# Performance work log

Hardware: AMD Instinct MI355X
Metric: run time of the kernel (lower is better)

The kernel has to match this reference:

```python
import jax, jax.numpy as jnp
import numpy as np

N_STEPS = 16
T_FINAL = 1.0


def setup_inputs() -> dict:
    key = jax.random.key(0)
    k = jax.random.split(key, 5)
    B, n, S = 131072, 8, 1
    return {
        "U0": jax.random.normal(k[0], (B, n, n), jnp.float32),
        "eps": jax.random.normal(k[1], (S, B, n, n), jnp.float32),
        "W0": 0.1 * jax.random.normal(k[2], (n, n), jnp.float32),
        "W1": 0.1 * jax.random.normal(k[3], (n, n), jnp.float32),
        "W2": 0.1 * jax.random.normal(k[4], (n, n), jnp.float32),
    }


def _alg_dyn(t, U, W0, W1, W2):
    # F(t, U; p) = antisym(W0 + t*W1 + U W2 U^T)  (real anti-Hermitian part)
    M = W0 + t * W1 + jnp.einsum('bij,jk,blk->bil', U, W2, U)
    return 0.5 * (M - jnp.swapaxes(M, -1, -2))


def _vel(t, U, W0, W1, W2):
    # dU/dt = F(t, U) @ U
    return _alg_dyn(t, U, W0, W1, W2) @ U


def _logj_rate(t, U, eps, W0, W1, W2):
    # Hutchinson estimator of tr(d vel / dU) per batch element: E_v[v . J v]
    f = lambda u: _vel(t, u, W0, W1, W2)

    def one(v):
        _, jv = jax.jvp(f, (U,), (v,))
        return jnp.sum(v * jv, axis=(-2, -1))  # [B]

    return jnp.mean(jax.vmap(one)(eps), axis=0)  # [B]


def reference(U0, eps, W0, W1, W2):
    dt = T_FINAL / N_STEPS

    def rhs(t, U):
        return _vel(t, U, W0, W1, W2), _logj_rate(t, U, eps, W0, W1, W2)

    def step(carry, i):
        U, lj = carry
        t = i.astype(U.dtype) * dt
        k1u, k1l = rhs(t, U)
        k2u, k2l = rhs(t + 0.5 * dt, U + 0.5 * dt * k1u)
        k3u, k3l = rhs(t + 0.5 * dt, U + 0.5 * dt * k2u)
        k4u, k4l = rhs(t + dt, U + dt * k3u)
        U = U + (dt / 6.0) * (k1u + 2.0 * k2u + 2.0 * k3u + k4u)
        lj = lj + (dt / 6.0) * (k1l + 2.0 * k2l + 2.0 * k3l + k4l)
        return (U, lj), None

    logj0 = jnp.zeros((U0.shape[0],), U0.dtype)
    (U, logj), _ = jax.lax.scan(step, (U0, logj0), jnp.arange(N_STEPS))
    return U, logj
```

## Files before the change

kernel.cpp:

```cpp
#include <hip/hip_runtime.h>
#include <stdint.h>

typedef unsigned int u32;
typedef unsigned short u16;
typedef float v2f __attribute__((ext_vector_type(2)));

#define NSTEP 16
#define DTS (1.0f/16.0f)

#define TAB_FLAG 0
#define TAB_W2   8
#define TAB_W2M  72
#define TAB_WT   136

__device__ __forceinline__ float b2f(u16 h){ return __uint_as_float(((u32)h) << 16); }
__device__ __forceinline__ u32 f2b(float f){
  u32 u = __float_as_uint(f);
  return (u + 0x7fffu + ((u >> 16) & 1u)) >> 16;
}
__host__ __device__ constexpr int TRI(int i, int j){ return i*7 - (i*(i-1))/2 + (j-i-1); }

__global__ void prep_kernel(const void* __restrict__ W0v, const void* __restrict__ W1v,
                            const void* __restrict__ W2v, float* __restrict__ ws)
{
  __shared__ int sflag;
  __shared__ float sW0[64], sW1[64], sW2[64];
  int t = threadIdx.x;

  if (t == 0) {
    const u16* w2h = (const u16*)W2v;
    int ok = 1;
    for (int x = 0; x < 64; ++x) {
      float v = b2f(w2h[x]);
      if (!(v > -1024.0f && v < 1024.0f)) { ok = 0; break; }
    }
    sflag = ok;
    ws[TAB_FLAG] = (float)ok;
  }
  __syncthreads();
  int isbf = sflag;

  if (t < 64) {
    if (isbf) {
      sW0[t] = b2f(((const u16*)W0v)[t]);
      sW1[t] = b2f(((const u16*)W1v)[t]);
      sW2[t] = b2f(((const u16*)W2v)[t]);
    } else {
      sW0[t] = ((const float*)W0v)[t];
      sW1[t] = ((const float*)W1v)[t];
      sW2[t] = ((const float*)W2v)[t];
    }
  }
  __syncthreads();

  if (t < 64) {
    int i = t >> 3, j = t & 7;
    ws[TAB_W2  + t] = sW2[t];
    ws[TAB_W2M + t] = sW2[t] - sW2[j*8+i];
  }
  for (int idx = t; idx < 64*28; idx += 256) {
    int s = idx / 28;
    int e = idx - s*28;
    int i = 0, r = e;
    while (r >= 7 - i) { r -= 7 - i; ++i; }
    int j = i + 1 + r;
    int step = s >> 2, st = s & 3;
    float toff = (st == 0) ? 0.0f : ((st == 3) ? 1.0f : 0.5f);
    float tt = ((float)step + toff) * DTS;
    float w0a = 0.5f*(sW0[i*8+j] - sW0[j*8+i]);
    float w1a = 0.5f*(sW1[i*8+j] - sW1[j*8+i]);
    ws[TAB_WT + s*32 + e] = fmaf(tt, w1a, w0a);
  }
}

#define SC(arr,i,k) (((k)&1) ? arr[(i)*4+((k)>>1)].y : arr[(i)*4+((k)>>1)].x)

__global__ void __attribute__((amdgpu_flat_work_group_size(256,256), amdgpu_waves_per_eu(1,1)))
flow_kernel(const void* __restrict__ U0v, const void* __restrict__ EPSv,
            const float* __restrict__ ws, void* __restrict__ outv, int B)
{
  int b = blockIdx.x * 256 + threadIdx.x;
  if (b >= B) return;
  const int isbf = (ws[TAB_FLAG] != 0.0f);

  v2f U2[32], V2[32], E2[32];
  if (isbf) {
    const uint4* pu = (const uint4*)((const u16*)U0v + (size_t)b*64);
    const uint4* pv = (const uint4*)((const u16*)EPSv + (size_t)b*64);
    #pragma unroll
    for (int q = 0; q < 8; ++q) {
      uint4 xu = pu[q];
      uint4 xv = pv[q];
      U2[4*q+0] = (v2f){b2f((u16)(xu.x&0xffffu)), b2f((u16)(xu.x>>16))};
      U2[4*q+1] = (v2f){b2f((u16)(xu.y&0xffffu)), b2f((u16)(xu.y>>16))};
      U2[4*q+2] = (v2f){b2f((u16)(xu.z&0xffffu)), b2f((u16)(xu.z>>16))};
      U2[4*q+3] = (v2f){b2f((u16)(xu.w&0xffffu)), b2f((u16)(xu.w>>16))};
      V2[4*q+0] = (v2f){b2f((u16)(xv.x&0xffffu)), b2f((u16)(xv.x>>16))};
      V2[4*q+1] = (v2f){b2f((u16)(xv.y&0xffffu)), b2f((u16)(xv.y>>16))};
      V2[4*q+2] = (v2f){b2f((u16)(xv.z&0xffffu)), b2f((u16)(xv.z>>16))};
      V2[4*q+3] = (v2f){b2f((u16)(xv.w&0xffffu)), b2f((u16)(xv.w>>16))};
    }
  } else {
    const float4* pu = (const float4*)((const float*)U0v + (size_t)b*64);
    const float4* pv = (const float4*)((const float*)EPSv + (size_t)b*64);
    #pragma unroll
    for (int q = 0; q < 16; ++q) {
      float4 xu = pu[q];
      float4 xv = pv[q];
      U2[2*q+0] = (v2f){xu.x, xu.y};  U2[2*q+1] = (v2f){xu.z, xu.w};
      V2[2*q+0] = (v2f){xv.x, xv.y};  V2[2*q+1] = (v2f){xv.z, xv.w};
    }
  }

  const v2f* W2p  = (const v2f*)(ws + TAB_W2);
  const v2f* W2mp = (const v2f*)(ws + TAB_W2M);

  #pragma unroll
  for (int i = 0; i < 8; ++i) {
    #pragma unroll
    for (int jp = 0; jp < 4; ++jp) {
      v2f a = SC(V2,i,0) * W2mp[0*4+jp];
      #pragma unroll
      for (int k = 1; k < 8; ++k) a += SC(V2,i,k) * W2mp[k*4+jp];
      E2[i*4+jp] = a;
    }
  }

  float lj = 0.0f;

  #pragma unroll 1
  for (int step = 0; step < NSTEP; ++step) {
    v2f Us2[32], acc2[32];
    #pragma unroll
    for (int x = 0; x < 32; ++x) { Us2[x] = U2[x]; acc2[x] = (v2f){0.0f, 0.0f}; }

    #pragma unroll 1
    for (int stage = 0; stage < 4; ++stage) {
      const float* wt = ws + TAB_WT + (size_t)(((step << 2) | stage) << 5);

      v2f A2[32];
      #pragma unroll
      for (int i = 0; i < 8; ++i) {
        #pragma unroll
        for (int jp = 0; jp < 4; ++jp) {
          v2f a = SC(U2,i,0) * W2p[0*4+jp];
          #pragma unroll
          for (int k = 1; k < 8; ++k) a += SC(U2,i,k) * W2p[k*4+jp];
          A2[i*4+jp] = a;
        }
      }

      float Fu[28];
      #pragma unroll
      for (int i = 0; i < 8; ++i) {
        #pragma unroll
        for (int j = i+1; j < 8; ++j) {
          v2f s2 = A2[i*4+0] * U2[j*4+0];
          #pragma unroll
          for (int kp = 1; kp < 4; ++kp) s2 += A2[i*4+kp] * U2[j*4+kp];
          #pragma unroll
          for (int kp = 0; kp < 4; ++kp) s2 -= A2[j*4+kp] * U2[i*4+kp];
          Fu[TRI(i,j)] = fmaf(0.5f, s2.x + s2.y, wt[TRI(i,j)]);
        }
      }

      float Ssum = 0.0f;
      #pragma unroll
      for (int i = 0; i < 8; ++i) {
        #pragma unroll
        for (int j = i+1; j < 8; ++j) {
          v2f d2 = V2[i*4+0] * U2[j*4+0];
          #pragma unroll
          for (int kp = 1; kp < 4; ++kp) d2 += V2[i*4+kp] * U2[j*4+kp];
          #pragma unroll
          for (int kp = 0; kp < 4; ++kp) d2 -= U2[i*4+kp] * V2[j*4+kp];
          v2f g2 = E2[i*4+0] * U2[j*4+0];
          #pragma unroll
          for (int kp = 1; kp < 4; ++kp) g2 += E2[i*4+kp] * U2[j*4+kp];
          #pragma unroll
          for (int kp = 0; kp < 4; ++kp) g2 -= E2[j*4+kp] * U2[i*4+kp];
          Ssum = fmaf(d2.x + d2.y, g2.x + g2.y, Ssum);
        }
      }
      float cl = (stage == 1 || stage == 2) ? (DTS/6.0f) : (DTS/12.0f);
      lj = fmaf(cl, Ssum, lj);

      float wa = (stage == 1 || stage == 2) ? 2.0f : 1.0f;
      #pragma unroll
      for (int i = 0; i < 8; ++i) {
        #pragma unroll
        for (int jp = 0; jp < 4; ++jp) {
          const int k0 = (i == 0) ? 1 : 0;
          float f0 = (i < k0) ? Fu[TRI(i<k0?i:k0, i<k0?k0:i)] : -Fu[TRI(i<k0?i:k0, i<k0?k0:i)];
          v2f s2 = f0 * U2[k0*4+jp];
          #pragma unroll
          for (int k = 0; k < 8; ++k) {
            if (k == i || k == k0) continue;
            float fk = (i < k) ? Fu[TRI(i<k?i:k, i<k?k:i)] : -Fu[TRI(i<k?i:k, i<k?k:i)];
            s2 += fk * U2[k*4+jp];
          }
          A2[i*4+jp] = s2;
          acc2[i*4+jp] += wa * s2;
        }
      }
      if (stage < 3) {
        float cs = (stage == 2) ? DTS : (0.5f*DTS);
        #pragma unroll
        for (int x = 0; x < 32; ++x) U2[x] = Us2[x] + cs * A2[x];
      }
    }

    #pragma unroll
    for (int x = 0; x < 32; ++x) U2[x] = Us2[x] + (DTS/6.0f) * acc2[x];
  }

  if (isbf) {
    u16* outU = (u16*)outv;
    uint4* po = (uint4*)(outU + (size_t)b*64);
    #pragma unroll
    for (int q = 0; q < 8; ++q) {
      uint4 o;
      o.x = f2b(U2[4*q+0].x) | (f2b(U2[4*q+0].y) << 16);
      o.y = f2b(U2[4*q+1].x) | (f2b(U2[4*q+1].y) << 16);
      o.z = f2b(U2[4*q+2].x) | (f2b(U2[4*q+2].y) << 16);
      o.w = f2b(U2[4*q+3].x) | (f2b(U2[4*q+3].y) << 16);
      po[q] = o;
    }
    outU[(size_t)B*64 + b] = (u16)f2b(lj);
  } else {
    float* outU = (float*)outv;
    float4* po = (float4*)(outU + (size_t)b*64);
    #pragma unroll
    for (int q = 0; q < 16; ++q) {
      float4 o;
      o.x = U2[2*q].x; o.y = U2[2*q].y; o.z = U2[2*q+1].x; o.w = U2[2*q+1].y;
      po[q] = o;
    }
    outU[(size_t)B*64 + b] = lj;
  }
}

extern "C" void kernel_launch(void* const* d_in, const int* in_sizes, int n_in,
                              void* d_out, int out_size, void* d_ws, size_t ws_size,
                              hipStream_t stream) {
  const void* U0  = d_in[0];
  const void* EPS = d_in[1];
  const void* W0  = d_in[2];
  const void* W1  = d_in[3];
  const void* W2  = d_in[4];
  float* ws = (float*)d_ws;
  int B = in_sizes[0] / 64;

  hipLaunchKernelGGL(prep_kernel, dim3(1), dim3(256), 0, stream, W0, W1, W2, ws);
  hipLaunchKernelGGL(flow_kernel, dim3((B + 255) / 256), dim3(256), 0, stream,
                     U0, EPS, ws, d_out, B);
}
```

Before: 629.2 us.

## Move V and E to LDS as bf16, restructure dots for register pressure

```diff
diff --git a/kernel.cpp b/kernel.cpp
--- a/kernel.cpp
+++ b/kernel.cpp
@@ -14,11 +14,22 @@
 #define TAB_WT   136
 
 __device__ __forceinline__ float b2f(u16 h){ return __uint_as_float(((u32)h) << 16); }
+__device__ __forceinline__ float bflo(u32 w){ return __uint_as_float(w << 16); }
+__device__ __forceinline__ float bfhi(u32 w){ return __uint_as_float(w & 0xffff0000u); }
 __device__ __forceinline__ u32 f2b(float f){
   u32 u = __float_as_uint(f);
   return (u + 0x7fffu + ((u >> 16) & 1u)) >> 16;
 }
 __host__ __device__ constexpr int TRI(int i, int j){ return i*7 - (i*(i-1))/2 + (j-i-1); }
+
+__device__ __forceinline__ v2f vfma(v2f a, v2f b, v2f c){ return __builtin_elementwise_fma(a, b, c); }
+__device__ __forceinline__ float dot8(const v2f* a, const v2f* u){
+  v2f d = a[0] * u[0];
+  d = vfma(a[1], u[1], d);
+  d = vfma(a[2], u[2], d);
+  d = vfma(a[3], u[3], d);
+  return d.x + d.y;
+}
 
 __global__ void prep_kernel(const void* __restrict__ W0v, const void* __restrict__ W1v,
                             const void* __restrict__ W2v, float* __restrict__ ws)
@@ -73,32 +84,57 @@
   }
 }
 
-#define SC(arr,i,k) (((k)&1) ? arr[(i)*4+((k)>>1)].y : arr[(i)*4+((k)>>1)].x)
-
-__global__ void __attribute__((amdgpu_flat_work_group_size(256,256), amdgpu_waves_per_eu(1,1)))
-flow_kernel(const void* __restrict__ U0v, const void* __restrict__ EPSv,
-            const float* __restrict__ ws, void* __restrict__ outv, int B)
+__global__ __launch_bounds__(256, 2) void flow_kernel(
+    const void* __restrict__ U0v, const void* __restrict__ EPSv,
+    const float* __restrict__ ws, void* __restrict__ outv, int B)
 {
-  int b = blockIdx.x * 256 + threadIdx.x;
+  __shared__ uint4 sV[8][256];
+  __shared__ uint4 sE[8][256];
+
+  const int tid = threadIdx.x;
+  const int b = blockIdx.x * 256 + tid;
   if (b >= B) return;
   const int isbf = (ws[TAB_FLAG] != 0.0f);
 
-  v2f U2[32], V2[32], E2[32];
+  const v2f* W2p = (const v2f*)(ws + TAB_W2);
+  const v2f* Mp  = (const v2f*)(ws + TAB_W2M);
+
+  v2f U2[32];
+
   if (isbf) {
     const uint4* pu = (const uint4*)((const u16*)U0v + (size_t)b*64);
     const uint4* pv = (const uint4*)((const u16*)EPSv + (size_t)b*64);
     #pragma unroll
     for (int q = 0; q < 8; ++q) {
       uint4 xu = pu[q];
-      uint4 xv = pv[q];
-      U2[4*q+0] = (v2f){b2f((u16)(xu.x&0xffffu)), b2f((u16)(xu.x>>16))};
-      U2[4*q+1] = (v2f){b2f((u16)(xu.y&0xffffu)), b2f((u16)(xu.y>>16))};
-      U2[4*q+2] = (v2f){b2f((u16)(xu.z&0xffffu)), b2f((u16)(xu.z>>16))};
-      U2[4*q+3] = (v2f){b2f((u16)(xu.w&0xffffu)), b2f((u16)(xu.w>>16))};
-      V2[4*q+0] = (v2f){b2f((u16)(xv.x&0xffffu)), b2f((u16)(xv.x>>16))};
-      V2[4*q+1] = (v2f){b2f((u16)(xv.y&0xffffu)), b2f((u16)(xv.y>>16))};
-      V2[4*q+2] = (v2f){b2f((u16)(xv.z&0xffffu)), b2f((u16)(xv.z>>16))};
-      V2[4*q+3] = (v2f){b2f((u16)(xv.w&0xffffu)), b2f((u16)(xv.w>>16))};
+      U2[4*q+0] = (v2f){bflo(xu.x), bfhi(xu.x)};
+      U2[4*q+1] = (v2f){bflo(xu.y), bfhi(xu.y)};
+      U2[4*q+2] = (v2f){bflo(xu.z), bfhi(xu.z)};
+      U2[4*q+3] = (v2f){bflo(xu.w), bfhi(xu.w)};
+    }
+    #pragma unroll
+    for (int r = 0; r < 8; ++r) {
+      uint4 xv = pv[r];
+      sV[r][tid] = xv;
+      v2f Vr2[4] = { (v2f){bflo(xv.x), bfhi(xv.x)}, (v2f){bflo(xv.y), bfhi(xv.y)},
+                     (v2f){bflo(xv.z), bfhi(xv.z)}, (v2f){bflo(xv.w), bfhi(xv.w)} };
+      v2f e[4];
+      #pragma unroll
+      for (int mp = 0; mp < 4; ++mp) {
+        v2f a = (v2f){Vr2[0].x, Vr2[0].x} * Mp[0*4+mp];
+        #pragma unroll
+        for (int k = 1; k < 8; ++k) {
+          float vk = (k & 1) ? Vr2[k>>1].y : Vr2[k>>1].x;
+          a = vfma((v2f){vk, vk}, Mp[k*4+mp], a);
+        }
+        e[mp] = a;
+      }
+      uint4 xe;
+      xe.x = f2b(e[0].x) | (f2b(e[0].y) << 16);
+      xe.y = f2b(e[1].x) | (f2b(e[1].y) << 16);
+      xe.z = f2b(e[2].x) | (f2b(e[2].y) << 16);
+      xe.w = f2b(e[3].x) | (f2b(e[3].y) << 16);
+      sE[r][tid] = xe;
     }
   } else {
     const float4* pu = (const float4*)((const float*)U0v + (size_t)b*64);
@@ -106,23 +142,35 @@
     #pragma unroll
     for (int q = 0; q < 16; ++q) {
       float4 xu = pu[q];
-      float4 xv = pv[q];
       U2[2*q+0] = (v2f){xu.x, xu.y};  U2[2*q+1] = (v2f){xu.z, xu.w};
-      V2[2*q+0] = (v2f){xv.x, xv.y};  V2[2*q+1] = (v2f){xv.z, xv.w};
-    }
-  }
-
-  const v2f* W2p  = (const v2f*)(ws + TAB_W2);
-  const v2f* W2mp = (const v2f*)(ws + TAB_W2M);
-
-  #pragma unroll
-  for (int i = 0; i < 8; ++i) {
-    #pragma unroll
-    for (int jp = 0; jp < 4; ++jp) {
-      v2f a = SC(V2,i,0) * W2mp[0*4+jp];
-      #pragma unroll
-      for (int k = 1; k < 8; ++k) a += SC(V2,i,k) * W2mp[k*4+jp];
-      E2[i*4+jp] = a;
+    }
+    #pragma unroll
+    for (int r = 0; r < 8; ++r) {
+      float4 a0 = pv[2*r], a1 = pv[2*r+1];
+      v2f Vr2[4] = { (v2f){a0.x, a0.y}, (v2f){a0.z, a0.w}, (v2f){a1.x, a1.y}, (v2f){a1.z, a1.w} };
+      uint4 xv;
+      xv.x = f2b(Vr2[0].x) | (f2b(Vr2[0].y) << 16);
+      xv.y = f2b(Vr2[1].x) | (f2b(Vr2[1].y) << 16);
+      xv.z = f2b(Vr2[2].x) | (f2b(Vr2[2].y) << 16);
+      xv.w = f2b(Vr2[3].x) | (f2b(Vr2[3].y) << 16);
+      sV[r][tid] = xv;
+      v2f e[4];
+      #pragma unroll
+      for (int mp = 0; mp < 4; ++mp) {
+        v2f a = (v2f){Vr2[0].x, Vr2[0].x} * Mp[0*4+mp];
+        #pragma unroll
+        for (int k = 1; k < 8; ++k) {
+          float vk = (k & 1) ? Vr2[k>>1].y : Vr2[k>>1].x;
+          a = vfma((v2f){vk, vk}, Mp[k*4+mp], a);
+        }
+        e[mp] = a;
+      }
+      uint4 xe;
+      xe.x = f2b(e[0].x) | (f2b(e[0].y) << 16);
+      xe.y = f2b(e[1].x) | (f2b(e[1].y) << 16);
+      xe.z = f2b(e[2].x) | (f2b(e[2].y) << 16);
+      xe.w = f2b(e[3].x) | (f2b(e[3].y) << 16);
+      sE[r][tid] = xe;
     }
   }
 
@@ -138,80 +186,84 @@
     for (int stage = 0; stage < 4; ++stage) {
       const float* wt = ws + TAB_WT + (size_t)(((step << 2) | stage) << 5);
 
-      v2f A2[32];
-      #pragma unroll
-      for (int i = 0; i < 8; ++i) {
-        #pragma unroll
-        for (int jp = 0; jp < 4; ++jp) {
-          v2f a = SC(U2,i,0) * W2p[0*4+jp];
-          #pragma unroll
-          for (int k = 1; k < 8; ++k) a += SC(U2,i,k) * W2p[k*4+jp];
-          A2[i*4+jp] = a;
-        }
-      }
-
-      float Fu[28];
-      #pragma unroll
-      for (int i = 0; i < 8; ++i) {
-        #pragma unroll
-        for (int j = i+1; j < 8; ++j) {
-          v2f s2 = A2[i*4+0] * U2[j*4+0];
-          #pragma unroll
-          for (int kp = 1; kp < 4; ++kp) s2 += A2[i*4+kp] * U2[j*4+kp];
-          #pragma unroll
-          for (int kp = 0; kp < 4; ++kp) s2 -= A2[j*4+kp] * U2[i*4+kp];
-          Fu[TRI(i,j)] = fmaf(0.5f, s2.x + s2.y, wt[TRI(i,j)]);
-        }
-      }
-
+      float Dp[28], Gp[28];
       float Ssum = 0.0f;
       #pragma unroll
-      for (int i = 0; i < 8; ++i) {
-        #pragma unroll
-        for (int j = i+1; j < 8; ++j) {
-          v2f d2 = V2[i*4+0] * U2[j*4+0];
-          #pragma unroll
-          for (int kp = 1; kp < 4; ++kp) d2 += V2[i*4+kp] * U2[j*4+kp];
-          #pragma unroll
-          for (int kp = 0; kp < 4; ++kp) d2 -= U2[i*4+kp] * V2[j*4+kp];
-          v2f g2 = E2[i*4+0] * U2[j*4+0];
-          #pragma unroll
-          for (int kp = 1; kp < 4; ++kp) g2 += E2[i*4+kp] * U2[j*4+kp];
-          #pragma unroll
-          for (int kp = 0; kp < 4; ++kp) g2 -= E2[j*4+kp] * U2[i*4+kp];
-          Ssum = fmaf(d2.x + d2.y, g2.x + g2.y, Ssum);
+      for (int r = 0; r < 8; ++r) {
+        uint4 xv = sV[r][tid];
+        uint4 xe = sE[r][tid];
+        v2f Vr2[4] = { (v2f){bflo(xv.x), bfhi(xv.x)}, (v2f){bflo(xv.y), bfhi(xv.y)},
+                       (v2f){bflo(xv.z), bfhi(xv.z)}, (v2f){bflo(xv.w), bfhi(xv.w)} };
+        v2f Er2[4] = { (v2f){bflo(xe.x), bfhi(xe.x)}, (v2f){bflo(xe.y), bfhi(xe.y)},
+                       (v2f){bflo(xe.z), bfhi(xe.z)}, (v2f){bflo(xe.w), bfhi(xe.w)} };
+        #pragma unroll
+        for (int j = 0; j < 8; ++j) {
+          if (j == r) continue;
+          float dv = dot8(Vr2, &U2[j*4]);
+          float de = dot8(Er2, &U2[j*4]);
+          if (j > r) {
+            Dp[TRI(r,j)] = dv;
+            Gp[TRI(r,j)] = de;
+          } else {
+            Ssum = fmaf(Dp[TRI(j,r)] - dv, Gp[TRI(j,r)] - de, Ssum);
+          }
         }
       }
       float cl = (stage == 1 || stage == 2) ? (DTS/6.0f) : (DTS/12.0f);
       lj = fmaf(cl, Ssum, lj);
 
+      float Fu[28];
+      #pragma unroll
+      for (int r = 0; r < 8; ++r) {
+        v2f Ar[4];
+        #pragma unroll
+        for (int jp = 0; jp < 4; ++jp) {
+          float u0 = U2[r*4].x;
+          v2f a = (v2f){u0, u0} * W2p[0*4+jp];
+          #pragma unroll
+          for (int k = 1; k < 8; ++k) {
+            float uk = (k & 1) ? U2[r*4 + (k>>1)].y : U2[r*4 + (k>>1)].x;
+            a = vfma((v2f){uk, uk}, W2p[k*4+jp], a);
+          }
+          Ar[jp] = a;
+        }
+        #pragma unroll
+        for (int j = 0; j < 8; ++j) {
+          if (j == r) continue;
+          float da = dot8(Ar, &U2[j*4]);
+          if (j > r) Fu[TRI(r,j)] = fmaf(0.5f, da, wt[TRI(r,j)]);
+          else       Fu[TRI(j,r)] = fmaf(-0.5f, da, Fu[TRI(j,r)]);
+        }
+      }
+
       float wa = (stage == 1 || stage == 2) ? 2.0f : 1.0f;
-      #pragma unroll
-      for (int i = 0; i < 8; ++i) {
-        #pragma unroll
-        for (int jp = 0; jp < 4; ++jp) {
+      float cs = (stage == 2) ? DTS : (0.5f*DTS);
+      #pragma unroll
+      for (int jp = 0; jp < 4; ++jp) {
+        v2f kc[8];
+        #pragma unroll
+        for (int i = 0; i < 8; ++i) {
           const int k0 = (i == 0) ? 1 : 0;
           float f0 = (i < k0) ? Fu[TRI(i<k0?i:k0, i<k0?k0:i)] : -Fu[TRI(i<k0?i:k0, i<k0?k0:i)];
-          v2f s2 = f0 * U2[k0*4+jp];
+          v2f s2 = (v2f){f0, f0} * U2[k0*4+jp];
           #pragma unroll
           for (int k = 0; k < 8; ++k) {
             if (k == i || k == k0) continue;
             float fk = (i < k) ? Fu[TRI(i<k?i:k, i<k?k:i)] : -Fu[TRI(i<k?i:k, i<k?k:i)];
-            s2 += fk * U2[k*4+jp];
+            s2 = vfma((v2f){fk, fk}, U2[k*4+jp], s2);
           }
-          A2[i*4+jp] = s2;
-          acc2[i*4+jp] += wa * s2;
-        }
-      }
-      if (stage < 3) {
-        float cs = (stage == 2) ? DTS : (0.5f*DTS);
-        #pragma unroll
-        for (int x = 0; x < 32; ++x) U2[x] = Us2[x] + cs * A2[x];
-      }
-    }
-
-    #pragma unroll
-    for (int x = 0; x < 32; ++x) U2[x] = Us2[x] + (DTS/6.0f) * acc2[x];
+          kc[i] = s2;
+        }
+        #pragma unroll
+        for (int i = 0; i < 8; ++i) {
+          acc2[i*4+jp] = vfma((v2f){wa, wa}, kc[i], acc2[i*4+jp]);
+          if (stage < 3) U2[i*4+jp] = vfma((v2f){cs, cs}, kc[i], Us2[i*4+jp]);
+        }
+      }
+    }
+
+    #pragma unroll
+    for (int x = 0; x < 32; ++x) U2[x] = vfma((v2f){DTS/6.0f, DTS/6.0f}, acc2[x], Us2[x]);
   }
 
   if (isbf) {
```

Measured after the change: 1.410 ms. +124.1%, slower.
